# Performance work log

Measured on AMD Instinct MI355X. Metric: run time of the kernel, lower is better.

## Reference

```python
import jax, jax.numpy as jnp
import numpy as np

HIDDEN = 512
HEADS = 8
HEAD_DIM = HIDDEN // HEADS


def setup_inputs() -> dict:
    key = jax.random.key(0)
    ks = jax.random.split(key, 13)
    B, S, H = 4, 2048, HIDDEN
    s = 1.0 / np.sqrt(H).astype(np.float32)
    inp = {
        "values": jax.random.normal(ks[0], (B, S, H), jnp.float32),
        "keys": jax.random.normal(ks[1], (B, S, H), jnp.float32),
        "query": jax.random.normal(ks[2], (B, S, H), jnp.float32),
        "mask": jax.random.randint(ks[3], (B, S), 0, 2, jnp.int32),
        "Wq": jax.random.normal(ks[4], (H, H), jnp.float32) * s,
        "bq": jnp.zeros((H,), jnp.float32),
        "Wk": jax.random.normal(ks[5], (H, H), jnp.float32) * s,
        "bk": jnp.zeros((H,), jnp.float32),
        "Wv": jax.random.normal(ks[6], (H, H), jnp.float32) * s,
        "bv": jnp.zeros((H,), jnp.float32),
        "Wo": jax.random.normal(ks[7], (H, H), jnp.float32) * s,
        "bo": jnp.zeros((H,), jnp.float32),
    }
    return inp


def reference(values, keys, query, mask, Wq, bq, Wk, bk, Wv, bv, Wo, bo):
    B, Sq, H = query.shape
    Sk = keys.shape[1]
    # projections (x @ W + b)
    Q = query @ Wq + bq
    K = keys @ Wk + bk
    V = values @ Wv + bv
    # [B, S, H] -> [B, heads, S, head_dim]
    def split(x, S):
        return x.reshape(B, S, HEADS, HEAD_DIM).transpose(0, 2, 1, 3)
    Qh, Kh, Vh = split(Q, Sq), split(K, Sk), split(V, Sk)
    scale = 1.0 / np.sqrt(HEAD_DIM).astype(np.float32)
    scores = jnp.einsum('bhqd,bhkd->bhqk', Qh, Kh) * scale  # [B,H,Sq,Sk]
    m = mask[:, None, None, :]  # [B,1,1,Sk]
    scores = jnp.where(m == 0, jnp.float32(-1e9), scores)
    attn = jax.nn.softmax(scores, axis=-1)
    ctx = jnp.einsum('bhqk,bhkd->bhqd', attn, Vh)
    ctx = ctx.transpose(0, 2, 1, 3).reshape(B, Sq, H)
    return ctx @ Wo + bo
```

## Files before the change

kernel.cpp:

```cpp
#include <hip/hip_runtime.h>

#define HID 512
#define NH 8
#define HD 64
#define BATCH 4
#define SEQ 2048
#define MTOT (BATCH * SEQ)

typedef unsigned short ushort_t;
typedef __bf16 bf16x8 __attribute__((ext_vector_type(8)));
typedef unsigned short ushort8v __attribute__((ext_vector_type(8)));
typedef unsigned short ushort4v __attribute__((ext_vector_type(4)));
typedef float floatx4 __attribute__((ext_vector_type(4)));
typedef unsigned int uintx4 __attribute__((ext_vector_type(4)));

static __device__ __forceinline__ unsigned short f2bf(float f) {
  __bf16 b = (__bf16)f;
  return __builtin_bit_cast(unsigned short, b);
}
static __device__ __forceinline__ float bf2f(unsigned short s) {
  union { unsigned int u; float f; } c; c.u = ((unsigned int)s) << 16;
  return c.f;
}
static __device__ __forceinline__ bf16x8 asbf(ushort8v v) {
  return __builtin_bit_cast(bf16x8, v);
}
static __device__ __forceinline__ float max3f(float a, float b, float c) {
  return fmaxf(fmaxf(a, b), c);
}
static __device__ __forceinline__ float fexp2(float x) {
  return __builtin_amdgcn_exp2f(x);
}
static __device__ __forceinline__ void gl_lds16(const ushort_t* g, ushort_t* l) {
  __builtin_amdgcn_global_load_lds(
      (const __attribute__((address_space(1))) void*)g,
      (__attribute__((address_space(3))) void*)l, 16, 0, 0);
}

#define SC_LOG2E 0.18033688011112042f

__global__ void detect_dtype(const unsigned int* __restrict__ q, int* __restrict__ flag) {
  if (threadIdx.x == 0 && blockIdx.x == 0) {
    int hits = 0;
    for (int i = 0; i < 256; ++i) {
      unsigned e = (q[i] >> 7) & 0xff;
      hits += (e >= 110 && e <= 136) ? 1 : 0;
    }
    flag[0] = (hits >= 128) ? 1 : 0;
  }
}

__global__ __launch_bounds__(256) void prep_w(
    const void* __restrict__ W0, const void* __restrict__ W1,
    const void* __restrict__ W2, const void* __restrict__ W3,
    ushort_t* __restrict__ T0, ushort_t* __restrict__ T1,
    ushort_t* __restrict__ T2, ushort_t* __restrict__ T3,
    const int* __restrict__ flag) {
  const int isbf = flag[0];
  const void* W; ushort_t* T;
  switch (blockIdx.y) {
    case 0: W = W0; T = T0; break;
    case 1: W = W1; T = T1; break;
    case 2: W = W2; T = T2; break;
    default: W = W3; T = T3; break;
  }
  int idx = blockIdx.x * 256 + threadIdx.x;
  int k = idx >> 9, n = idx & 511;
  ushort_t v = isbf ? ((const ushort_t*)W)[k * HID + n]
                    : f2bf(((const float*)W)[k * HID + n]);
  T[n * HID + k] = v;
}

__global__ __launch_bounds__(256) void prep_b(
    const void* __restrict__ B0, const void* __restrict__ B1,
    const void* __restrict__ B2, const void* __restrict__ B3,
    float* __restrict__ biasF, const int* __restrict__ flag) {
  const int isbf = flag[0];
  int i = blockIdx.x * 256 + threadIdx.x;
  int t = i >> 9, j = i & 511;
  const void* B = (t == 0) ? B0 : (t == 1) ? B1 : (t == 2) ? B2 : B3;
  biasF[i] = isbf ? bf2f(((const ushort_t*)B)[j]) : ((const float*)B)[j];
}

__global__ __launch_bounds__(256) void prep_mask(
    const int* __restrict__ mask, float* __restrict__ mb) {
  int i = blockIdx.x * 256 + threadIdx.x;
  mb[i] = mask[i] ? 0.f : -1e9f;
}

__global__ __launch_bounds__(256) void prep_x(
    const void* __restrict__ X0, const void* __restrict__ X1,
    const void* __restrict__ X2, ushort_t* __restrict__ Xb,
    const int* __restrict__ flag) {
  const int isbf = flag[0];
  const int z = blockIdx.y;
  const void* X = (z == 0) ? X0 : (z == 1) ? X1 : X2;
  long i = (long)(blockIdx.x * 256 + threadIdx.x) * 8;
  ushort8v o;
  if (isbf) {
    o = *(const ushort8v*)((const ushort_t*)X + i);
  } else {
    floatx4 f0 = *(const floatx4*)((const float*)X + i);
    floatx4 f1 = *(const floatx4*)((const float*)X + i + 4);
#pragma unroll
    for (int r = 0; r < 4; ++r) { o[r] = f2bf(f0[r]); o[4 + r] = f2bf(f1[r]); }
  }
  *(ushort8v*)(Xb + (size_t)z * MTOT * HID + i) = o;
}

__global__ __launch_bounds__(256) void gemm_qkv2(
    const ushort_t* __restrict__ Xb, const ushort_t* __restrict__ WtBase,
    const float* __restrict__ biasBase, ushort_t* __restrict__ YBase) {
  const int z = blockIdx.z;
  const ushort_t* X = Xb + (size_t)z * MTOT * HID;
  const ushort_t* Wt = WtBase + (size_t)z * HID * HID;
  const float* biasF = biasBase + (size_t)z * HID;
  ushort_t* Y = YBase + (size_t)z * MTOT * HID;

  const int tid = threadIdx.x;
  const int wid = tid >> 6, lane = tid & 63;
  const int id = lane & 15, quad = lane >> 4;
  const int wm = wid >> 1, wn = wid & 1;
  const int m0 = blockIdx.x * 128, n0 = blockIdx.y * 128;

  __shared__ ushort_t As[128 * 64];
  __shared__ ushort_t Bs[128 * 64];

  const int lrow = lane >> 3;
  const int scb  = (lane & 7) ^ lrow;

  floatx4 acc[4][4];
#pragma unroll
  for (int i = 0; i < 4; ++i)
#pragma unroll
    for (int j = 0; j < 4; ++j) acc[i][j] = (floatx4){0.f, 0.f, 0.f, 0.f};

  for (int k0 = 0; k0 < HID; k0 += 64) {
    __syncthreads();
#pragma unroll
    for (int i = 0; i < 4; ++i) {
      int r = wid * 32 + i * 8 + lrow;
      gl_lds16(X + (long)(m0 + r) * HID + k0 + scb * 8, &As[(wid * 32 + i * 8) * 64]);
    }
#pragma unroll
    for (int i = 0; i < 4; ++i) {
      int r = wid * 32 + i * 8 + lrow;
      gl_lds16(Wt + (long)(n0 + r) * HID + k0 + scb * 8, &Bs[(wid * 32 + i * 8) * 64]);
    }
    __syncthreads();
#pragma unroll
    for (int kk = 0; kk < 64; kk += 32) {
      ushort8v af[4], bfv[4];
      const int cb = (kk >> 3) + quad;
#pragma unroll
      for (int ms = 0; ms < 4; ++ms) {
        int row = wm * 64 + ms * 16 + id;
        af[ms] = *(const ushort8v*)(&As[row * 64 + ((cb ^ (id & 7)) << 3)]);
      }
#pragma unroll
      for (int ns = 0; ns < 4; ++ns) {
        int row = wn * 64 + ns * 16 + id;
        bfv[ns] = *(const ushort8v*)(&Bs[row * 64 + ((cb ^ (id & 7)) << 3)]);
      }
#pragma unroll
      for (int ms = 0; ms < 4; ++ms)
#pragma unroll
        for (int ns = 0; ns < 4; ++ns)
          acc[ms][ns] = __builtin_amdgcn_mfma_f32_16x16x32_bf16(asbf(af[ms]), asbf(bfv[ns]), acc[ms][ns], 0, 0, 0);
    }
  }
#pragma unroll
  for (int ns = 0; ns < 4; ++ns) {
    int col = n0 + wn * 64 + ns * 16 + id;
    float bv = biasF[col];
#pragma unroll
    for (int ms = 0; ms < 4; ++ms) {
      int row0 = m0 + wm * 64 + ms * 16 + quad * 4;
#pragma unroll
      for (int r = 0; r < 4; ++r)
        Y[(long)(row0 + r) * HID + col] = f2bf(acc[ms][ns][r] + bv);
    }
  }
}

__global__ __launch_bounds__(256) void gemm_out2(
    const ushort_t* __restrict__ X, const ushort_t* __restrict__ Wt,
    const float* __restrict__ biasF, void* __restrict__ out,
    const int* __restrict__ flag) {
  const int isbf = flag[0];
  const int tid = threadIdx.x;
  const int wid = tid >> 6, lane = tid & 63;
  const int id = lane & 15, quad = lane >> 4;
  const int wm = wid >> 1, wn = wid & 1;
  const int m0 = blockIdx.x * 64, n0 = blockIdx.y * 128;

  __shared__ ushort_t As[64 * 64];
  __shared__ ushort_t Bs[128 * 64];

  const int lrow = lane >> 3;
  const int scb  = (lane & 7) ^ lrow;

  floatx4 acc[2][4];
#pragma unroll
  for (int i = 0; i < 2; ++i)
#pragma unroll
    for (int j = 0; j < 4; ++j) acc[i][j] = (floatx4){0.f, 0.f, 0.f, 0.f};

  for (int k0 = 0; k0 < HID; k0 += 64) {
    __syncthreads();
#pragma unroll
    for (int i = 0; i < 2; ++i) {
      int r = wid * 16 + i * 8 + lrow;
      gl_lds16(X + (long)(m0 + r) * HID + k0 + scb * 8, &As[(wid * 16 + i * 8) * 64]);
    }
#pragma unroll
    for (int i = 0; i < 4; ++i) {
      int r = wid * 32 + i * 8 + lrow;
      gl_lds16(Wt + (long)(n0 + r) * HID + k0 + scb * 8, &Bs[(wid * 32 + i * 8) * 64]);
    }
    __syncthreads();
#pragma unroll
    for (int kk = 0; kk < 64; kk += 32) {
      ushort8v af[2], bfv[4];
      const int cb = (kk >> 3) + quad;
#pragma unroll
      for (int ms = 0; ms < 2; ++ms) {
        int row = wm * 32 + ms * 16 + id;
        af[ms] = *(const ushort8v*)(&As[row * 64 + ((cb ^ (id & 7)) << 3)]);
      }
#pragma unroll
      for (int ns = 0; ns < 4; ++ns) {
        int row = wn * 64 + ns * 16 + id;
        bfv[ns] = *(const ushort8v*)(&Bs[row * 64 + ((cb ^ (id & 7)) << 3)]);
      }
#pragma unroll
      for (int ms = 0; ms < 2; ++ms)
#pragma unroll
        for (int ns = 0; ns < 4; ++ns)
          acc[ms][ns] = __builtin_amdgcn_mfma_f32_16x16x32_bf16(asbf(af[ms]), asbf(bfv[ns]), acc[ms][ns], 0, 0, 0);
    }
  }
#pragma unroll
  for (int ns = 0; ns < 4; ++ns) {
    int col = n0 + wn * 64 + ns * 16 + id;
    float bv = biasF[col];
#pragma unroll
    for (int ms = 0; ms < 2; ++ms) {
      int row0 = m0 + wm * 32 + ms * 16 + quad * 4;
      if (isbf) {
        ushort_t* o = (ushort_t*)out;
#pragma unroll
        for (int r = 0; r < 4; ++r) o[(long)(row0 + r) * HID + col] = f2bf(acc[ms][ns][r] + bv);
      } else {
        float* o = (float*)out;
#pragma unroll
        for (int r = 0; r < 4; ++r) o[(long)(row0 + r) * HID + col] = acc[ms][ns][r] + bv;
      }
    }
  }
}

__global__ __launch_bounds__(256) void flash_attn(
    const ushort_t* __restrict__ Q, const ushort_t* __restrict__ K,
    const ushort_t* __restrict__ V, const float* __restrict__ mb,
    ushort_t* __restrict__ ctx) {
  const int qblk = blockIdx.x, h = blockIdx.y, b = blockIdx.z;
  const int tid = threadIdx.x;
  const int wid = tid >> 6, lane = tid & 63;
  const int id = lane & 15, quad = lane >> 4;

  __shared__ ushort_t Kt[64 * 72];
  __shared__ ushort_t Vt[64 * 72];
  __shared__ ushort_t Pl[4][32 * 72];

  const ushort_t* Qb = Q + (long)(b * SEQ + qblk * 128 + wid * 32) * HID + h * HD;
  const ushort_t* Kb = K + (long)(b * SEQ) * HID + h * HD;
  const ushort_t* Vb = V + (long)(b * SEQ) * HID + h * HD;
  const float* mrow = mb + b * SEQ;

  ushort8v qf[2][2];
#pragma unroll
  for (int qs = 0; qs < 2; ++qs)
#pragma unroll
    for (int kh = 0; kh < 2; ++kh)
      qf[qs][kh] = *(const ushort8v*)(Qb + (qs * 16 + id) * HID + kh * 32 + quad * 8);

  floatx4 o[4][2];
  float m_i[2] = {-1e30f, -1e30f}, l_i[2] = {0.f, 0.f};
#pragma unroll
  for (int dg = 0; dg < 4; ++dg) { o[dg][0] = (floatx4){0,0,0,0}; o[dg][1] = (floatx4){0,0,0,0}; }

  const int skey = tid >> 2;
  const int sdc  = (tid & 3) * 16;
  const int vkp  = (tid & 31) * 2;
  const int vdc  = (tid >> 5) * 8;

  ushort8v k0v, k1v, v0v, v1v;
  {
    const ushort_t* kpp = Kb + (long)skey * HID + sdc;
    k0v = *(const ushort8v*)(kpp);
    k1v = *(const ushort8v*)(kpp + 8);
    const ushort_t* vp0 = Vb + (long)vkp * HID + vdc;
    v0v = *(const ushort8v*)(vp0);
    v1v = *(const ushort8v*)(vp0 + HID);
  }

  for (int kb = 0; kb < SEQ / 64; ++kb) {
    *(ushort8v*)(&Kt[skey * 72 + sdc])     = k0v;
    *(ushort8v*)(&Kt[skey * 72 + sdc + 8]) = k1v;
    {
      uintx4 a = __builtin_bit_cast(uintx4, v0v);
      uintx4 bq = __builtin_bit_cast(uintx4, v1v);
#pragma unroll
      for (int j = 0; j < 4; ++j) {
        unsigned int d0 = __builtin_amdgcn_perm(bq[j], a[j], 0x05040100u);
        unsigned int d1 = __builtin_amdgcn_perm(bq[j], a[j], 0x07060302u);
        *(unsigned int*)(&Vt[(vdc + 2 * j) * 72 + vkp])     = d0;
        *(unsigned int*)(&Vt[(vdc + 2 * j + 1) * 72 + vkp]) = d1;
      }
    }
    __syncthreads();

    if (kb + 1 < SEQ / 64) {
      const ushort_t* kpp = Kb + (long)((kb + 1) * 64 + skey) * HID + sdc;
      k0v = *(const ushort8v*)(kpp);
      k1v = *(const ushort8v*)(kpp + 8);
      const ushort_t* vp0 = Vb + (long)((kb + 1) * 64 + vkp) * HID + vdc;
      v0v = *(const ushort8v*)(vp0);
      v1v = *(const ushort8v*)(vp0 + HID);
    }

    floatx4 st[2][4];
#pragma unroll
    for (int ks = 0; ks < 4; ++ks) {
      ushort8v kf0 = *(const ushort8v*)(&Kt[(ks * 16 + id) * 72 + quad * 8]);
      ushort8v kf1 = *(const ushort8v*)(&Kt[(ks * 16 + id) * 72 + 32 + quad * 8]);
#pragma unroll
      for (int qs = 0; qs < 2; ++qs) {
        floatx4 a = (floatx4){0,0,0,0};
        a = __builtin_amdgcn_mfma_f32_16x16x32_bf16(asbf(kf0), asbf(qf[qs][0]), a, 0, 0, 0);
        a = __builtin_amdgcn_mfma_f32_16x16x32_bf16(asbf(kf1), asbf(qf[qs][1]), a, 0, 0, 0);
        st[qs][ks] = a;
      }
    }
#pragma unroll
    for (int ks = 0; ks < 4; ++ks) {
      floatx4 mbv = *(const floatx4*)(mrow + kb * 64 + ks * 16 + quad * 4);
#pragma unroll
      for (int r = 0; r < 4; ++r) {
        st[0][ks][r] = fmaf(st[0][ks][r], SC_LOG2E, mbv[r]);
        st[1][ks][r] = fmaf(st[1][ks][r], SC_LOG2E, mbv[r]);
      }
    }
#pragma unroll
    for (int qs = 0; qs < 2; ++qs) {
      float a0 = max3f(st[qs][0][0], st[qs][0][1], st[qs][0][2]);
      float a1 = max3f(st[qs][0][3], st[qs][1][0], st[qs][1][1]);
      float a2 = max3f(st[qs][1][2], st[qs][1][3], st[qs][2][0]);
      float a3 = max3f(st[qs][2][1], st[qs][2][2], st[qs][2][3]);
      float a4 = max3f(st[qs][3][0], st[qs][3][1], st[qs][3][2]);
      float mx = max3f(a0, a1, st[qs][3][3]);
      float mz = max3f(a2, a3, a4);
      mx = fmaxf(mx, mz);
      mx = fmaxf(mx, __shfl_xor(mx, 16));
      mx = fmaxf(mx, __shfl_xor(mx, 32));
      if (!__all(mx - m_i[qs] <= 8.f)) {
        float mnew = fmaxf(m_i[qs], mx);
        float alpha = fexp2(m_i[qs] - mnew);
        m_i[qs] = mnew;
        l_i[qs] *= alpha;
#pragma unroll
        for (int dg = 0; dg < 4; ++dg) o[dg][qs] *= alpha;
      }
      float mcur = m_i[qs];
      floatx4 rsv = (floatx4){0.f, 0.f, 0.f, 0.f};
#pragma unroll
      for (int ks = 0; ks < 4; ++ks) {
        ushort4v pk;
#pragma unroll
        for (int r = 0; r < 4; ++r) {
          float p = fexp2(st[qs][ks][r] - mcur);
          rsv[r] += p;
          pk[r] = f2bf(p);
        }
        *(ushort4v*)(&Pl[wid][(qs * 16 + id) * 72 + ks * 16 + quad * 4]) = pk;
      }
      float rs = (rsv[0] + rsv[1]) + (rsv[2] + rsv[3]);
      rs += __shfl_xor(rs, 16);
      rs += __shfl_xor(rs, 32);
      l_i[qs] += rs;
    }

#pragma unroll
    for (int kc = 0; kc < 2; ++kc) {
      ushort8v pf0 = *(const ushort8v*)(&Pl[wid][(0 * 16 + id) * 72 + kc * 32 + quad * 8]);
      ushort8v pf1 = *(const ushort8v*)(&Pl[wid][(1 * 16 + id) * 72 + kc * 32 + quad * 8]);
#pragma unroll
      for (int dg = 0; dg < 4; ++dg) {
        ushort8v vf = *(const ushort8v*)(&Vt[(dg * 16 + id) * 72 + kc * 32 + quad * 8]);
        o[dg][0] = __builtin_amdgcn_mfma_f32_16x16x32_bf16(asbf(vf), asbf(pf0), o[dg][0], 0, 0, 0);
        o[dg][1] = __builtin_amdgcn_mfma_f32_16x16x32_bf16(asbf(vf), asbf(pf1), o[dg][1], 0, 0, 0);
      }
    }
    __syncthreads();
  }

#pragma unroll
  for (int qs = 0; qs < 2; ++qs) {
    float inv = 1.0f / l_i[qs];
    long qrow = (long)(b * SEQ + qblk * 128 + wid * 32 + qs * 16 + id);
#pragma unroll
    for (int dg = 0; dg < 4; ++dg) {
      ushort4v pk;
#pragma unroll
      for (int r = 0; r < 4; ++r) pk[r] = f2bf(o[dg][qs][r] * inv);
      *(ushort4v*)(&ctx[qrow * HID + h * HD + dg * 16 + quad * 4]) = pk;
    }
  }
}

extern "C" void kernel_launch(void* const* d_in, const int* in_sizes, int n_in,
                              void* d_out, int out_size, void* d_ws, size_t ws_size,
                              hipStream_t stream) {
  const void* values = d_in[0];
  const void* keys   = d_in[1];
  const void* query  = d_in[2];
  const int*  mask   = (const int*)d_in[3];
  const void* Wq = d_in[4];  const void* bq = d_in[5];
  const void* Wk = d_in[6];  const void* bk = d_in[7];
  const void* Wv = d_in[8];  const void* bv = d_in[9];
  const void* Wo = d_in[10]; const void* bo = d_in[11];

  ushort_t* ws = (ushort_t*)d_ws;
  const size_t NEL = (size_t)MTOT * HID;
  ushort_t* Qp  = ws;
  ushort_t* Kp  = ws + NEL;
  ushort_t* Vp  = ws + 2 * NEL;
  ushort_t* Cp  = ws + 3 * NEL;
  ushort_t* Xb  = ws + 4 * NEL;
  ushort_t* WqT = ws + 7 * NEL;
  ushort_t* WkT = WqT + (size_t)HID * HID;
  ushort_t* WvT = WkT + (size_t)HID * HID;
  ushort_t* WoT = WvT + (size_t)HID * HID;
  float* biasF  = (float*)(WoT + (size_t)HID * HID);
  float* mbias  = biasF + 4 * HID;
  int* flag     = (int*)(mbias + (size_t)BATCH * SEQ);

  detect_dtype<<<1, 64, 0, stream>>>((const unsigned int*)query, flag);
  prep_w<<<dim3(1024, 4), 256, 0, stream>>>(Wq, Wk, Wv, Wo, WqT, WkT, WvT, WoT, flag);
  prep_b<<<8, 256, 0, stream>>>(bq, bk, bv, bo, biasF, flag);
  prep_mask<<<MTOT / 256, 256, 0, stream>>>(mask, mbias);
  prep_x<<<dim3(MTOT * HID / (256 * 8), 3), 256, 0, stream>>>(query, keys, values, Xb, flag);

  gemm_qkv2<<<dim3(MTOT / 128, HID / 128, 3), 256, 0, stream>>>(Xb, WqT, biasF, Qp);

  flash_attn<<<dim3(SEQ / 128, NH, BATCH), 256, 0, stream>>>(Qp, Kp, Vp, mbias, Cp);

  gemm_out2<<<dim3(MTOT / 64, HID / 128), 256, 0, stream>>>(
      Cp, WoT, biasF + 3 * HID, d_out, flag);
}
```

Baseline: 231.3 us.

## Fuse input cast into QKV GEMM, tile weight transpose, widen attention blocks

The separate prep_x cast kernel is removed, and the QKV projection now reads fp32 or bf16 inputs directly, converting them to bf16 while staging into shared memory. Each block computes a 32-row by full-512-column tile, with a swizzled block order. The weight transpose now goes through a shared-memory tile so reads and writes are coalesced. Flash attention moves to 512 threads with 16 query rows per wave, splits K and V staging across the two thread halves, adds s_setprio around the MFMA sections and swizzles block order, trading fewer registers per wave for more waves.

```diff
diff --git a/kernel.cpp b/kernel.cpp
--- a/kernel.cpp
+++ b/kernel.cpp
@@ -64,11 +64,41 @@
     case 2: W = W2; T = T2; break;
     default: W = W3; T = T3; break;
   }
-  int idx = blockIdx.x * 256 + threadIdx.x;
-  int k = idx >> 9, n = idx & 511;
-  ushort_t v = isbf ? ((const ushort_t*)W)[k * HID + n]
-                    : f2bf(((const float*)W)[k * HID + n]);
-  T[n * HID + k] = v;
+  __shared__ ushort_t Ts[64 * 72];
+  const int tid = threadIdx.x;
+  const int kt = (blockIdx.x >> 3) * 64;
+  const int nt = (blockIdx.x & 7) * 64;
+  const int r = tid >> 2;
+  const int c = (tid & 3) * 16;
+
+  ushort8v v0, v1;
+  if (isbf) {
+    const ushort_t* p = (const ushort_t*)W + (long)(kt + r) * HID + nt + c;
+    v0 = *(const ushort8v*)(p);
+    v1 = *(const ushort8v*)(p + 8);
+  } else {
+    const float* p = (const float*)W + (long)(kt + r) * HID + nt + c;
+    floatx4 f0 = *(const floatx4*)(p);
+    floatx4 f1 = *(const floatx4*)(p + 4);
+    floatx4 f2 = *(const floatx4*)(p + 8);
+    floatx4 f3 = *(const floatx4*)(p + 12);
+#pragma unroll
+    for (int i = 0; i < 4; ++i) {
+      v0[i] = f2bf(f0[i]); v0[4 + i] = f2bf(f1[i]);
+      v1[i] = f2bf(f2[i]); v1[4 + i] = f2bf(f3[i]);
+    }
+  }
+  *(ushort8v*)(&Ts[r * 72 + c])     = v0;
+  *(ushort8v*)(&Ts[r * 72 + c + 8]) = v1;
+  __syncthreads();
+  ushort8v o0, o1;
+#pragma unroll
+  for (int j = 0; j < 8; ++j) o0[j] = Ts[(c + j) * 72 + r];
+#pragma unroll
+  for (int j = 0; j < 8; ++j) o1[j] = Ts[(c + 8 + j) * 72 + r];
+  ushort_t* q = T + (long)(nt + r) * HID + kt + c;
+  *(ushort8v*)(q)     = o0;
+  *(ushort8v*)(q + 8) = o1;
 }
 
 __global__ __launch_bounds__(256) void prep_b(
@@ -88,31 +118,16 @@
   mb[i] = mask[i] ? 0.f : -1e9f;
 }
 
-__global__ __launch_bounds__(256) void prep_x(
-    const void* __restrict__ X0, const void* __restrict__ X1,
-    const void* __restrict__ X2, ushort_t* __restrict__ Xb,
-    const int* __restrict__ flag) {
+__global__ __launch_bounds__(256) void gemm_qkv3(
+    const void* __restrict__ X0, const void* __restrict__ X1, const void* __restrict__ X2,
+    const ushort_t* __restrict__ WtBase, const float* __restrict__ biasBase,
+    ushort_t* __restrict__ YBase, const int* __restrict__ flag) {
   const int isbf = flag[0];
-  const int z = blockIdx.y;
+  int lin = blockIdx.x + 256 * blockIdx.z;
+  int swz = (lin & 7) * 96 + (lin >> 3);
+  const int z = swz >> 8;
+  const int mblk = swz & 255;
   const void* X = (z == 0) ? X0 : (z == 1) ? X1 : X2;
-  long i = (long)(blockIdx.x * 256 + threadIdx.x) * 8;
-  ushort8v o;
-  if (isbf) {
-    o = *(const ushort8v*)((const ushort_t*)X + i);
-  } else {
-    floatx4 f0 = *(const floatx4*)((const float*)X + i);
-    floatx4 f1 = *(const floatx4*)((const float*)X + i + 4);
-#pragma unroll
-    for (int r = 0; r < 4; ++r) { o[r] = f2bf(f0[r]); o[4 + r] = f2bf(f1[r]); }
-  }
-  *(ushort8v*)(Xb + (size_t)z * MTOT * HID + i) = o;
-}
-
-__global__ __launch_bounds__(256) void gemm_qkv2(
-    const ushort_t* __restrict__ Xb, const ushort_t* __restrict__ WtBase,
-    const float* __restrict__ biasBase, ushort_t* __restrict__ YBase) {
-  const int z = blockIdx.z;
-  const ushort_t* X = Xb + (size_t)z * MTOT * HID;
   const ushort_t* Wt = WtBase + (size_t)z * HID * HID;
   const float* biasF = biasBase + (size_t)z * HID;
   ushort_t* Y = YBase + (size_t)z * MTOT * HID;
@@ -120,62 +135,65 @@
   const int tid = threadIdx.x;
   const int wid = tid >> 6, lane = tid & 63;
   const int id = lane & 15, quad = lane >> 4;
-  const int wm = wid >> 1, wn = wid & 1;
-  const int m0 = blockIdx.x * 128, n0 = blockIdx.y * 128;
-
-  __shared__ ushort_t As[128 * 64];
-  __shared__ ushort_t Bs[128 * 64];
-
-  const int lrow = lane >> 3;
-  const int scb  = (lane & 7) ^ lrow;
-
-  floatx4 acc[4][4];
-#pragma unroll
-  for (int i = 0; i < 4; ++i)
-#pragma unroll
-    for (int j = 0; j < 4; ++j) acc[i][j] = (floatx4){0.f, 0.f, 0.f, 0.f};
-
-  for (int k0 = 0; k0 < HID; k0 += 64) {
-    __syncthreads();
-#pragma unroll
-    for (int i = 0; i < 4; ++i) {
-      int r = wid * 32 + i * 8 + lrow;
-      gl_lds16(X + (long)(m0 + r) * HID + k0 + scb * 8, &As[(wid * 32 + i * 8) * 64]);
-    }
-#pragma unroll
-    for (int i = 0; i < 4; ++i) {
-      int r = wid * 32 + i * 8 + lrow;
-      gl_lds16(Wt + (long)(n0 + r) * HID + k0 + scb * 8, &Bs[(wid * 32 + i * 8) * 64]);
-    }
-    __syncthreads();
-#pragma unroll
-    for (int kk = 0; kk < 64; kk += 32) {
-      ushort8v af[4], bfv[4];
-      const int cb = (kk >> 3) + quad;
-#pragma unroll
-      for (int ms = 0; ms < 4; ++ms) {
-        int row = wm * 64 + ms * 16 + id;
-        af[ms] = *(const ushort8v*)(&As[row * 64 + ((cb ^ (id & 7)) << 3)]);
-      }
-#pragma unroll
-      for (int ns = 0; ns < 4; ++ns) {
-        int row = wn * 64 + ns * 16 + id;
-        bfv[ns] = *(const ushort8v*)(&Bs[row * 64 + ((cb ^ (id & 7)) << 3)]);
-      }
-#pragma unroll
-      for (int ms = 0; ms < 4; ++ms)
-#pragma unroll
-        for (int ns = 0; ns < 4; ++ns)
+  const int m0 = mblk * 32;
+
+  __shared__ ushort_t As[32 * 32];
+  __shared__ ushort_t Bs[512 * 32];
+
+  const int a_r = tid >> 3;
+  const int a_b = (tid & 7) >> 1;
+  const int a_o = (tid & 1) * 4;
+  const int a_pb = a_b ^ (a_r & 3);
+  const int b_ro = lane >> 2;
+  const int b_scb = (lane & 3);
+
+  floatx4 acc[2][8];
+#pragma unroll
+  for (int i = 0; i < 2; ++i)
+#pragma unroll
+    for (int j = 0; j < 8; ++j) acc[i][j] = (floatx4){0.f, 0.f, 0.f, 0.f};
+
+  for (int k0 = 0; k0 < HID; k0 += 32) {
+    ushort4v aW;
+    if (isbf) {
+      aW = *(const ushort4v*)((const ushort_t*)X + (long)(m0 + a_r) * HID + k0 + (tid & 7) * 4);
+    } else {
+      floatx4 f = *(const floatx4*)((const float*)X + (long)(m0 + a_r) * HID + k0 + (tid & 7) * 4);
+#pragma unroll
+      for (int i = 0; i < 4; ++i) aW[i] = f2bf(f[i]);
+    }
+    __syncthreads();
+    *(ushort4v*)(&As[a_r * 32 + (a_pb << 3) + a_o]) = aW;
+#pragma unroll
+    for (int i = 0; i < 8; ++i) {
+      int rb = wid * 128 + i * 16;
+      int srow = rb + b_ro;
+      gl_lds16(Wt + (long)srow * HID + k0 + ((b_scb ^ (srow & 3)) << 3), &Bs[rb * 32]);
+    }
+    __syncthreads();
+    {
+      ushort8v af[2], bfv[8];
+      const int pb = (quad ^ (id & 3)) << 3;
+#pragma unroll
+      for (int ms = 0; ms < 2; ++ms)
+        af[ms] = *(const ushort8v*)(&As[(ms * 16 + id) * 32 + pb]);
+#pragma unroll
+      for (int ns = 0; ns < 8; ++ns)
+        bfv[ns] = *(const ushort8v*)(&Bs[(wid * 128 + ns * 16 + id) * 32 + pb]);
+#pragma unroll
+      for (int ms = 0; ms < 2; ++ms)
+#pragma unroll
+        for (int ns = 0; ns < 8; ++ns)
           acc[ms][ns] = __builtin_amdgcn_mfma_f32_16x16x32_bf16(asbf(af[ms]), asbf(bfv[ns]), acc[ms][ns], 0, 0, 0);
     }
   }
 #pragma unroll
-  for (int ns = 0; ns < 4; ++ns) {
-    int col = n0 + wn * 64 + ns * 16 + id;
+  for (int ns = 0; ns < 8; ++ns) {
+    int col = wid * 128 + ns * 16 + id;
     float bv = biasF[col];
 #pragma unroll
-    for (int ms = 0; ms < 4; ++ms) {
-      int row0 = m0 + wm * 64 + ms * 16 + quad * 4;
+    for (int ms = 0; ms < 2; ++ms) {
+      int row0 = m0 + ms * 16 + quad * 4;
 #pragma unroll
       for (int r = 0; r < 4; ++r)
         Y[(long)(row0 + r) * HID + col] = f2bf(acc[ms][ns][r] + bv);
@@ -260,57 +278,61 @@
   }
 }
 
-__global__ __launch_bounds__(256) void flash_attn(
+__global__ __launch_bounds__(512) void flash_attn(
     const ushort_t* __restrict__ Q, const ushort_t* __restrict__ K,
     const ushort_t* __restrict__ V, const float* __restrict__ mb,
     ushort_t* __restrict__ ctx) {
-  const int qblk = blockIdx.x, h = blockIdx.y, b = blockIdx.z;
+  int lin = blockIdx.x + 16 * blockIdx.y + 128 * blockIdx.z;
+  int swz = (lin & 7) * 64 + (lin >> 3);
+  const int qblk = swz & 15, h = (swz >> 4) & 7, b = swz >> 7;
   const int tid = threadIdx.x;
   const int wid = tid >> 6, lane = tid & 63;
   const int id = lane & 15, quad = lane >> 4;
 
   __shared__ ushort_t Kt[64 * 72];
   __shared__ ushort_t Vt[64 * 72];
-  __shared__ ushort_t Pl[4][32 * 72];
-
-  const ushort_t* Qb = Q + (long)(b * SEQ + qblk * 128 + wid * 32) * HID + h * HD;
+  __shared__ ushort_t Pl[8][16 * 72];
+
+  const ushort_t* Qb = Q + (long)(b * SEQ + qblk * 128 + wid * 16) * HID + h * HD;
   const ushort_t* Kb = K + (long)(b * SEQ) * HID + h * HD;
   const ushort_t* Vb = V + (long)(b * SEQ) * HID + h * HD;
   const float* mrow = mb + b * SEQ;
 
-  ushort8v qf[2][2];
-#pragma unroll
-  for (int qs = 0; qs < 2; ++qs)
-#pragma unroll
-    for (int kh = 0; kh < 2; ++kh)
-      qf[qs][kh] = *(const ushort8v*)(Qb + (qs * 16 + id) * HID + kh * 32 + quad * 8);
-
-  floatx4 o[4][2];
-  float m_i[2] = {-1e30f, -1e30f}, l_i[2] = {0.f, 0.f};
-#pragma unroll
-  for (int dg = 0; dg < 4; ++dg) { o[dg][0] = (floatx4){0,0,0,0}; o[dg][1] = (floatx4){0,0,0,0}; }
-
-  const int skey = tid >> 2;
-  const int sdc  = (tid & 3) * 16;
-  const int vkp  = (tid & 31) * 2;
-  const int vdc  = (tid >> 5) * 8;
-
-  ushort8v k0v, k1v, v0v, v1v;
-  {
+  ushort8v qf[2];
+#pragma unroll
+  for (int kh = 0; kh < 2; ++kh)
+    qf[kh] = *(const ushort8v*)(Qb + id * HID + kh * 32 + quad * 8);
+
+  floatx4 o[4];
+  float m_i = -1e30f, l_i = 0.f;
+#pragma unroll
+  for (int dg = 0; dg < 4; ++dg) o[dg] = (floatx4){0, 0, 0, 0};
+
+  const bool kstager = (tid < 256);
+  const int t2 = tid & 255;
+  const int skey = t2 >> 2;
+  const int sdc  = (t2 & 3) * 16;
+  const int vkp  = (t2 & 31) * 2;
+  const int vdc  = (t2 >> 5) * 8;
+
+  ushort8v r0, r1;
+  if (kstager) {
     const ushort_t* kpp = Kb + (long)skey * HID + sdc;
-    k0v = *(const ushort8v*)(kpp);
-    k1v = *(const ushort8v*)(kpp + 8);
+    r0 = *(const ushort8v*)(kpp);
+    r1 = *(const ushort8v*)(kpp + 8);
+  } else {
     const ushort_t* vp0 = Vb + (long)vkp * HID + vdc;
-    v0v = *(const ushort8v*)(vp0);
-    v1v = *(const ushort8v*)(vp0 + HID);
+    r0 = *(const ushort8v*)(vp0);
+    r1 = *(const ushort8v*)(vp0 + HID);
   }
 
   for (int kb = 0; kb < SEQ / 64; ++kb) {
-    *(ushort8v*)(&Kt[skey * 72 + sdc])     = k0v;
-    *(ushort8v*)(&Kt[skey * 72 + sdc + 8]) = k1v;
-    {
-      uintx4 a = __builtin_bit_cast(uintx4, v0v);
-      uintx4 bq = __builtin_bit_cast(uintx4, v1v);
+    if (kstager) {
+      *(ushort8v*)(&Kt[skey * 72 + sdc])     = r0;
+      *(ushort8v*)(&Kt[skey * 72 + sdc + 8]) = r1;
+    } else {
+      uintx4 a = __builtin_bit_cast(uintx4, r0);
+      uintx4 bq = __builtin_bit_cast(uintx4, r1);
 #pragma unroll
       for (int j = 0; j < 4; ++j) {
         unsigned int d0 = __builtin_amdgcn_perm(bq[j], a[j], 0x05040100u);
@@ -322,98 +344,96 @@
     __syncthreads();
 
     if (kb + 1 < SEQ / 64) {
-      const ushort_t* kpp = Kb + (long)((kb + 1) * 64 + skey) * HID + sdc;
-      k0v = *(const ushort8v*)(kpp);
-      k1v = *(const ushort8v*)(kpp + 8);
-      const ushort_t* vp0 = Vb + (long)((kb + 1) * 64 + vkp) * HID + vdc;
-      v0v = *(const ushort8v*)(vp0);
-      v1v = *(const ushort8v*)(vp0 + HID);
-    }
-
-    floatx4 st[2][4];
+      if (kstager) {
+        const ushort_t* kpp = Kb + (long)((kb + 1) * 64 + skey) * HID + sdc;
+        r0 = *(const ushort8v*)(kpp);
+        r1 = *(const ushort8v*)(kpp + 8);
+      } else {
+        const ushort_t* vp0 = Vb + (long)((kb + 1) * 64 + vkp) * HID + vdc;
+        r0 = *(const ushort8v*)(vp0);
+        r1 = *(const ushort8v*)(vp0 + HID);
+      }
+    }
+
+    floatx4 st[4];
+    __builtin_amdgcn_s_setprio(1);
 #pragma unroll
     for (int ks = 0; ks < 4; ++ks) {
       ushort8v kf0 = *(const ushort8v*)(&Kt[(ks * 16 + id) * 72 + quad * 8]);
       ushort8v kf1 = *(const ushort8v*)(&Kt[(ks * 16 + id) * 72 + 32 + quad * 8]);
-#pragma unroll
-      for (int qs = 0; qs < 2; ++qs) {
-        floatx4 a = (floatx4){0,0,0,0};
-        a = __builtin_amdgcn_mfma_f32_16x16x32_bf16(asbf(kf0), asbf(qf[qs][0]), a, 0, 0, 0);
-        a = __builtin_amdgcn_mfma_f32_16x16x32_bf16(asbf(kf1), asbf(qf[qs][1]), a, 0, 0, 0);
-        st[qs][ks] = a;
-      }
-    }
+      floatx4 a = (floatx4){0, 0, 0, 0};
+      a = __builtin_amdgcn_mfma_f32_16x16x32_bf16(asbf(kf0), asbf(qf[0]), a, 0, 0, 0);
+      a = __builtin_amdgcn_mfma_f32_16x16x32_bf16(asbf(kf1), asbf(qf[1]), a, 0, 0, 0);
+      st[ks] = a;
+    }
+    __builtin_amdgcn_s_setprio(0);
 #pragma unroll
     for (int ks = 0; ks < 4; ++ks) {
       floatx4 mbv = *(const floatx4*)(mrow + kb * 64 + ks * 16 + quad * 4);
 #pragma unroll
-      for (int r = 0; r < 4; ++r) {
-        st[0][ks][r] = fmaf(st[0][ks][r], SC_LOG2E, mbv[r]);
-        st[1][ks][r] = fmaf(st[1][ks][r], SC_LOG2E, mbv[r]);
-      }
-    }
-#pragma unroll
-    for (int qs = 0; qs < 2; ++qs) {
-      float a0 = max3f(st[qs][0][0], st[qs][0][1], st[qs][0][2]);
-      float a1 = max3f(st[qs][0][3], st[qs][1][0], st[qs][1][1]);
-      float a2 = max3f(st[qs][1][2], st[qs][1][3], st[qs][2][0]);
-      float a3 = max3f(st[qs][2][1], st[qs][2][2], st[qs][2][3]);
-      float a4 = max3f(st[qs][3][0], st[qs][3][1], st[qs][3][2]);
-      float mx = max3f(a0, a1, st[qs][3][3]);
-      float mz = max3f(a2, a3, a4);
+      for (int r = 0; r < 4; ++r)
+        st[ks][r] = fmaf(st[ks][r], SC_LOG2E, mbv[r]);
+    }
+    {
+      float t0 = max3f(st[0][0], st[0][1], st[0][2]);
+      float t1 = max3f(st[0][3], st[1][0], st[1][1]);
+      float t2m = max3f(st[1][2], st[1][3], st[2][0]);
+      float t3 = max3f(st[2][1], st[2][2], st[2][3]);
+      float t4 = max3f(st[3][0], st[3][1], st[3][2]);
+      float mx = max3f(t0, t1, st[3][3]);
+      float mz = max3f(t2m, t3, t4);
       mx = fmaxf(mx, mz);
       mx = fmaxf(mx, __shfl_xor(mx, 16));
       mx = fmaxf(mx, __shfl_xor(mx, 32));
-      if (!__all(mx - m_i[qs] <= 8.f)) {
-        float mnew = fmaxf(m_i[qs], mx);
-        float alpha = fexp2(m_i[qs] - mnew);
-        m_i[qs] = mnew;
-        l_i[qs] *= alpha;
-#pragma unroll
-        for (int dg = 0; dg < 4; ++dg) o[dg][qs] *= alpha;
-      }
-      float mcur = m_i[qs];
+      if (!__all(mx - m_i <= 8.f)) {
+        float mnew = fmaxf(m_i, mx);
+        float alpha = fexp2(m_i - mnew);
+        m_i = mnew;
+        l_i *= alpha;
+#pragma unroll
+        for (int dg = 0; dg < 4; ++dg) o[dg] *= alpha;
+      }
+      float mcur = m_i;
       floatx4 rsv = (floatx4){0.f, 0.f, 0.f, 0.f};
 #pragma unroll
       for (int ks = 0; ks < 4; ++ks) {
         ushort4v pk;
 #pragma unroll
         for (int r = 0; r < 4; ++r) {
-          float p = fexp2(st[qs][ks][r] - mcur);
+          float p = fexp2(st[ks][r] - mcur);
           rsv[r] += p;
           pk[r] = f2bf(p);
         }
-        *(ushort4v*)(&Pl[wid][(qs * 16 + id) * 72 + ks * 16 + quad * 4]) = pk;
+        *(ushort4v*)(&Pl[wid][id * 72 + ks * 16 + quad * 4]) = pk;
       }
       float rs = (rsv[0] + rsv[1]) + (rsv[2] + rsv[3]);
       rs += __shfl_xor(rs, 16);
       rs += __shfl_xor(rs, 32);
-      l_i[qs] += rs;
-    }
-
+      l_i += rs;
+    }
+
+    __builtin_amdgcn_s_setprio(1);
 #pragma unroll
     for (int kc = 0; kc < 2; ++kc) {
-      ushort8v pf0 = *(const ushort8v*)(&Pl[wid][(0 * 16 + id) * 72 + kc * 32 + quad * 8]);
-      ushort8v pf1 = *(const ushort8v*)(&Pl[wid][(1 * 16 + id) * 72 + kc * 32 + quad * 8]);
+      ushort8v pf = *(const ushort8v*)(&Pl[wid][id * 72 + kc * 32 + quad * 8]);
 #pragma unroll
       for (int dg = 0; dg < 4; ++dg) {
         ushort8v vf = *(const ushort8v*)(&Vt[(dg * 16 + id) * 72 + kc * 32 + quad * 8]);
-        o[dg][0] = __builtin_amdgcn_mfma_f32_16x16x32_bf16(asbf(vf), asbf(pf0), o[dg][0], 0, 0, 0);
-        o[dg][1] = __builtin_amdgcn_mfma_f32_16x16x32_bf16(asbf(vf), asbf(pf1), o[dg][1], 0, 0, 0);
-      }
-    }
-    __syncthreads();
-  }
-
-#pragma unroll
-  for (int qs = 0; qs < 2; ++qs) {
-    float inv = 1.0f / l_i[qs];
-    long qrow = (long)(b * SEQ + qblk * 128 + wid * 32 + qs * 16 + id);
+        o[dg] = __builtin_amdgcn_mfma_f32_16x16x32_bf16(asbf(vf), asbf(pf), o[dg], 0, 0, 0);
+      }
+    }
+    __builtin_amdgcn_s_setprio(0);
+    __syncthreads();
+  }
+
+  {
+    float inv = 1.0f / l_i;
+    long qrow = (long)(b * SEQ + qblk * 128 + wid * 16 + id);
 #pragma unroll
     for (int dg = 0; dg < 4; ++dg) {
       ushort4v pk;
 #pragma unroll
-      for (int r = 0; r < 4; ++r) pk[r] = f2bf(o[dg][qs][r] * inv);
+      for (int r = 0; r < 4; ++r) pk[r] = f2bf(o[dg][r] * inv);
       *(ushort4v*)(&ctx[qrow * HID + h * HD + dg * 16 + quad * 4]) = pk;
     }
   }
@@ -437,8 +457,7 @@
   ushort_t* Kp  = ws + NEL;
   ushort_t* Vp  = ws + 2 * NEL;
   ushort_t* Cp  = ws + 3 * NEL;
-  ushort_t* Xb  = ws + 4 * NEL;
-  ushort_t* WqT = ws + 7 * NEL;
+  ushort_t* WqT = ws + 4 * NEL;
   ushort_t* WkT = WqT + (size_t)HID * HID;
   ushort_t* WvT = WkT + (size_t)HID * HID;
   ushort_t* WoT = WvT + (size_t)HID * HID;
@@ -447,14 +466,14 @@
   int* flag     = (int*)(mbias + (size_t)BATCH * SEQ);
 
   detect_dtype<<<1, 64, 0, stream>>>((const unsigned int*)query, flag);
-  prep_w<<<dim3(1024, 4), 256, 0, stream>>>(Wq, Wk, Wv, Wo, WqT, WkT, WvT, WoT, flag);
+  prep_w<<<dim3(64, 4), 256, 0, stream>>>(Wq, Wk, Wv, Wo, WqT, WkT, WvT, WoT, flag);
   prep_b<<<8, 256, 0, stream>>>(bq, bk, bv, bo, biasF, flag);
   prep_mask<<<MTOT / 256, 256, 0, stream>>>(mask, mbias);
-  prep_x<<<dim3(MTOT * HID / (256 * 8), 3), 256, 0, stream>>>(query, keys, values, Xb, flag);
-
-  gemm_qkv2<<<dim3(MTOT / 128, HID / 128, 3), 256, 0, stream>>>(Xb, WqT, biasF, Qp);
-
-  flash_attn<<<dim3(SEQ / 128, NH, BATCH), 256, 0, stream>>>(Qp, Kp, Vp, mbias, Cp);
+
+  gemm_qkv3<<<dim3(MTOT / 32, 1, 3), 256, 0, stream>>>(
+      query, keys, values, WqT, biasF, Qp, flag);
+
+  flash_attn<<<dim3(SEQ / 128, NH, BATCH), 512, 0, stream>>>(Qp, Kp, Vp, mbias, Cp);
 
   gemm_out2<<<dim3(MTOT / 64, HID / 128), 256, 0, stream>>>(
       Cp, WoT, biasF + 3 * HID, d_out, flag);
```

New measurement: 235.7 us. No clear change (+1.9%).
